# Kernel optimization log

Measured on AMD Instinct MI355X. Metric: run time of the kernel, lower is better.

Reference implementation:

```python
import jax, jax.numpy as jnp
import numpy as np

NEI = 15  # module hard-codes 15 neighbors per node via reshape(N, 15, 2)


def setup_inputs() -> dict:
    N = 10000
    # 15-regular symmetric circulant graph: offsets +-1..+-7 and +N/2 (its own inverse).
    offsets = np.array(list(range(1, 8)) + list(range(-7, 0)) + [N // 2], dtype=np.int64)
    cols = (np.arange(N)[:, None] + offsets[None, :]) % N  # (N, 15)
    adj = np.zeros((N, N), dtype=np.float32)
    adj[np.repeat(np.arange(N), NEI), cols.ravel()] = 1.0
    return {"adjacency_matrix": jnp.asarray(adj)}


def reference(adjacency_matrix):
    N = adjacency_matrix.shape[0]
    # Exactly 15 nonzeros per row -> static size N*15; row-major order matches
    # torch .nonzero(), so reshape gives per-row neighbor columns.
    _, cols = jnp.nonzero(adjacency_matrix, size=N * NEI)
    nb1 = cols.reshape(N, NEI)            # (N,15)   neighbors_one_indexes
    nb2 = nb1[nb1]                        # (N,15,15)  neighbors_two_indexes
    nb3 = nb1[nb2]                        # (N,15,15,15) neighbors_three_indexes
    # closed 3-walk: l-th neighbor of k equals the start node i
    closed = nb3 == jnp.arange(N)[:, None, None, None]
    i, j, k, l = jnp.nonzero(closed)      # data-dependent count (eager)
    # triangles_indexes_test[:, :3] == (i, nb1[i,j], nb2[i,j,k]); temp_l is dropped
    tri = jnp.stack((i, nb1[i, j], nb2[i, j, k]), axis=1)
    tri_sorted = jnp.sort(tri, axis=-1)
    triangles_ids_igraph = jnp.unique(tri_sorted, axis=0)
    return triangles_ids_igraph
```

## Files before the change

### kernel.cpp

```cpp
#include <hip/hip_runtime.h>
#include <math.h>

#define NEI 15
#define ROWSTRIDE 16

typedef float f4 __attribute__((ext_vector_type(4)));

#define GET16(n0, n1, n2, n3, K)                                   \
    ((K) < 8                                                       \
         ? ((K) < 4                                                \
                ? ((K) == 0 ? (n0).x : (K) == 1 ? (n0).y           \
                                : (K) == 2 ? (n0).z : (n0).w)      \
                : ((K) == 4 ? (n1).x : (K) == 5 ? (n1).y           \
                                : (K) == 6 ? (n1).z : (n1).w))     \
         : ((K) < 12                                               \
                ? ((K) == 8 ? (n2).x : (K) == 9 ? (n2).y           \
                                : (K) == 10 ? (n2).z : (n2).w)     \
                : ((K) == 12 ? (n3).x : (K) == 13 ? (n3).y         \
                                : (K) == 14 ? (n3).z : (n3).w)))

__device__ __forceinline__ int mbcnt64(unsigned long long m) {
    int c = __builtin_amdgcn_mbcnt_lo((unsigned)m, 0);
    c = __builtin_amdgcn_mbcnt_hi((unsigned)(m >> 32), c);
    return c;
}

__global__ void find_nb_kernel(const float* __restrict__ A,
                               int* __restrict__ nb, int N, int totalWaves) {
    const int wavesPerBlock = blockDim.x >> 6;
    const int waveId = blockIdx.x * wavesPerBlock + (threadIdx.x >> 6);
    const int lane = threadIdx.x & 63;
    const int n4 = N >> 2;

    for (int row = waveId; row < N; row += totalWaves) {
        const f4* rowp = reinterpret_cast<const f4*>(A + (long long)row * N);
        int count = 0;

        for (int c0 = 0; c0 < n4; c0 += 256) {
            const int i0 = c0 + lane;
            const int i1 = i0 + 64, i2 = i0 + 128, i3 = i0 + 192;
            f4 v0 = {0.f, 0.f, 0.f, 0.f}, v1 = {0.f, 0.f, 0.f, 0.f};
            f4 v2 = {0.f, 0.f, 0.f, 0.f}, v3 = {0.f, 0.f, 0.f, 0.f};
            if (i0 < n4) v0 = __builtin_nontemporal_load(&rowp[i0]);
            if (i1 < n4) v1 = __builtin_nontemporal_load(&rowp[i1]);
            if (i2 < n4) v2 = __builtin_nontemporal_load(&rowp[i2]);
            if (i3 < n4) v3 = __builtin_nontemporal_load(&rowp[i3]);

            const bool a0 = (v0.x != 0.f) || (v0.y != 0.f) || (v0.z != 0.f) || (v0.w != 0.f);
            const bool a1 = (v1.x != 0.f) || (v1.y != 0.f) || (v1.z != 0.f) || (v1.w != 0.f);
            const bool a2 = (v2.x != 0.f) || (v2.y != 0.f) || (v2.z != 0.f) || (v2.w != 0.f);
            const bool a3 = (v3.x != 0.f) || (v3.y != 0.f) || (v3.z != 0.f) || (v3.w != 0.f);
            if (__ballot(a0 || a1 || a2 || a3) == 0ull) continue;

            #pragma unroll
            for (int q = 0; q < 4; ++q) {
                const f4 v = (q == 0) ? v0 : (q == 1) ? v1 : (q == 2) ? v2 : v3;
                const int idx = c0 + q * 64 + lane;
                const unsigned long long m0 = __ballot(v.x != 0.f);
                const unsigned long long m1 = __ballot(v.y != 0.f);
                const unsigned long long m2 = __ballot(v.z != 0.f);
                const unsigned long long m3 = __ballot(v.w != 0.f);
                if ((m0 | m1 | m2 | m3) != 0ull) {
                    const int below = mbcnt64(m0) + mbcnt64(m1) + mbcnt64(m2) + mbcnt64(m3);
                    const int b0 = (int)((m0 >> lane) & 1ull);
                    const int b1 = (int)((m1 >> lane) & 1ull);
                    const int b2 = (int)((m2 >> lane) & 1ull);
                    const int base = count + below;
                    if (v.x != 0.f) { const int p = base;                if (p < NEI) nb[row * ROWSTRIDE + p] = (idx << 2) + 0; }
                    if (v.y != 0.f) { const int p = base + b0;           if (p < NEI) nb[row * ROWSTRIDE + p] = (idx << 2) + 1; }
                    if (v.z != 0.f) { const int p = base + b0 + b1;      if (p < NEI) nb[row * ROWSTRIDE + p] = (idx << 2) + 2; }
                    if (v.w != 0.f) { const int p = base + b0 + b1 + b2; if (p < NEI) nb[row * ROWSTRIDE + p] = (idx << 2) + 3; }
                    count += __popcll(m0) + __popcll(m1) + __popcll(m2) + __popcll(m3);
                }
            }
        }
        const int base4 = n4 << 2;
        const int rem = N - base4;
        if (rem > 0) {
            float v = 0.f;
            if (lane < rem) v = A[(long long)row * N + base4 + lane];
            const unsigned long long m = __ballot(v != 0.f);
            if (v != 0.f) {
                const int p = count + mbcnt64(m);
                if (p < NEI) nb[row * ROWSTRIDE + p] = base4 + lane;
            }
        }
    }
}

__global__ void count_tri_kernel(const int* __restrict__ nb,
                                 int* __restrict__ mask2,
                                 int* __restrict__ offs2,
                                 int* __restrict__ blockSums, int N) {
    __shared__ int partial[256];
    const int tid = blockIdx.x * 256 + threadIdx.x;
    const int M = N * NEI;
    int c = 0, mask = 0;
    if (tid < M) {
        const int i = tid / NEI;
        const int j = tid - i * NEI;
        const int a = nb[i * ROWSTRIDE + j];
        if (a > i) {
            const int4* np = reinterpret_cast<const int4*>(nb + a * ROWSTRIDE);
            const int4 n0 = np[0], n1 = np[1], n2 = np[2], n3 = np[3];
            const int4* vp = reinterpret_cast<const int4*>(nb + i * ROWSTRIDE);
            const int4 w0 = vp[0], w1 = vp[1], w2 = vp[2], w3 = vp[3];
            #pragma unroll
            for (int k = 1; k < NEI; ++k) {
                if (k > j) {
                    const int b = GET16(w0, w1, w2, w3, k);
                    const bool adj =
                        (n0.x == b) || (n0.y == b) || (n0.z == b) || (n0.w == b) ||
                        (n1.x == b) || (n1.y == b) || (n1.z == b) || (n1.w == b) ||
                        (n2.x == b) || (n2.y == b) || (n2.z == b) || (n2.w == b) ||
                        (n3.x == b) || (n3.y == b) || (n3.z == b);
                    if (adj) { mask |= (1 << k); ++c; }
                }
            }
        }
        mask2[tid] = mask;
    }
    partial[threadIdx.x] = c;
    __syncthreads();
    #pragma unroll
    for (int d = 1; d < 256; d <<= 1) {
        const int mine  = partial[threadIdx.x];
        const int other = (threadIdx.x >= d) ? partial[threadIdx.x - d] : 0;
        __syncthreads();
        partial[threadIdx.x] = mine + other;
        __syncthreads();
    }
    if (tid < M) offs2[tid] = (threadIdx.x == 0) ? 0 : partial[threadIdx.x - 1];
    if (threadIdx.x == 255) blockSums[blockIdx.x] = partial[255];
}

__global__ void scan2_kernel(const int* __restrict__ blockSums,
                             int* __restrict__ blockOffs, int B) {
    __shared__ int partial[256];
    const int tid = threadIdx.x;
    const int per = (B + 255) / 256;
    const int start = tid * per;
    int s = 0;
    for (int q = 0; q < per; ++q) {
        const int idx = start + q;
        if (idx < B) s += blockSums[idx];
    }
    partial[tid] = s;
    __syncthreads();
    #pragma unroll
    for (int d = 1; d < 256; d <<= 1) {
        const int mine  = partial[tid];
        const int other = (tid >= d) ? partial[tid - d] : 0;
        __syncthreads();
        partial[tid] = mine + other;
        __syncthreads();
    }
    int run = (tid == 0) ? 0 : partial[tid - 1];
    for (int q = 0; q < per; ++q) {
        const int idx = start + q;
        if (idx < B) { blockOffs[idx] = run; run += blockSums[idx]; }
    }
}

__global__ void emit_tri_kernel(const int* __restrict__ nb,
                                const int* __restrict__ mask2,
                                const int* __restrict__ offs2,
                                const int* __restrict__ blockOffs,
                                int* __restrict__ out, int N) {
    const int tid = blockIdx.x * blockDim.x + threadIdx.x;
    const int M = N * NEI;
    if (tid >= M) return;
    const int mask = mask2[tid];
    if (mask == 0) return;
    const int i = tid / NEI;
    const int j = tid - i * NEI;
    const int a = nb[i * ROWSTRIDE + j];
    const int4* vp = reinterpret_cast<const int4*>(nb + i * ROWSTRIDE);
    const int4 w0 = vp[0], w1 = vp[1], w2 = vp[2], w3 = vp[3];
    int pos = offs2[tid] + blockOffs[tid >> 8];
    #pragma unroll
    for (int k = 1; k < NEI; ++k) {
        if ((mask >> k) & 1) {
            const int b = GET16(w0, w1, w2, w3, k);
            out[3 * pos + 0] = i;
            out[3 * pos + 1] = a;
            out[3 * pos + 2] = b;
            ++pos;
        }
    }
}

extern "C" void kernel_launch(void* const* d_in, const int* in_sizes, int n_in,
                              void* d_out, int out_size, void* d_ws, size_t ws_size,
                              hipStream_t stream) {
    const float* A = (const float*)d_in[0];
    const long long total = (long long)in_sizes[0];
    const int N = (int)llround(sqrt((double)total));
    const int M = N * NEI;
    const int B = (M + 255) / 256;

    int* ws = (int*)d_ws;
    int* w_nb    = ws;
    int* w_mask2 = ws + N * ROWSTRIDE;
    int* w_offs2 = w_mask2 + M;
    int* w_bsum  = w_offs2 + M;
    int* w_boff  = w_bsum + B;

    int* out = (int*)d_out;

    {
        int totalWaves = (N <= 8192) ? N : (N + 1) / 2;
        const int blocks = (totalWaves + 3) / 4;
        totalWaves = blocks * 4;
        find_nb_kernel<<<blocks, 256, 0, stream>>>(A, w_nb, N, totalWaves);
    }
    count_tri_kernel<<<B, 256, 0, stream>>>(w_nb, w_mask2, w_offs2, w_bsum, N);
    scan2_kernel<<<1, 256, 0, stream>>>(w_bsum, w_boff, B);
    {
        const int threads = 256;
        const int blocks = (M + threads - 1) / threads;
        emit_tri_kernel<<<blocks, threads, 0, stream>>>(w_nb, w_mask2, w_offs2, w_boff, out, N);
    }
}
```

Measured before the change: 76.89 us.

## Fuse count, scan and emit into one single-pass decoupled-lookback kernel

Replaces the separate count, block-scan and emit kernels with one kernel. It computes per-block triangle counts, resolves the global offset with a decoupled lookback over per-block status flags, then writes triangles directly from registers. Flag state is zeroed inside the first kernel. This removes two launches and the mask and offset round-trips through global memory. In exchange, blocks spin waiting on their predecessors, which relies on blocks being scheduled in order.

```diff
diff --git a/kernel.cpp b/kernel.cpp
--- a/kernel.cpp
+++ b/kernel.cpp
@@ -3,6 +3,10 @@
 
 #define NEI 15
 #define ROWSTRIDE 16
+
+#define FLAG_INVALID 0
+#define FLAG_AGG     1
+#define FLAG_PREFIX  2
 
 typedef float f4 __attribute__((ext_vector_type(4)));
 
@@ -26,7 +30,12 @@
 }
 
 __global__ void find_nb_kernel(const float* __restrict__ A,
-                               int* __restrict__ nb, int N, int totalWaves) {
+                               int* __restrict__ nb,
+                               int* __restrict__ state, int nState,
+                               int N, int totalWaves) {
+    if (blockIdx.x == 0) {
+        for (int q = threadIdx.x; q < nState; q += blockDim.x) state[q] = 0;
+    }
     const int wavesPerBlock = blockDim.x >> 6;
     const int waveId = blockIdx.x * wavesPerBlock + (threadIdx.x >> 6);
     const int lane = threadIdx.x & 63;
@@ -88,23 +97,25 @@
     }
 }
 
-__global__ void count_tri_kernel(const int* __restrict__ nb,
-                                 int* __restrict__ mask2,
-                                 int* __restrict__ offs2,
-                                 int* __restrict__ blockSums, int N) {
+__global__ __launch_bounds__(256) void tri_kernel(const int* __restrict__ nb,
+                                                  int* __restrict__ state,
+                                                  int* __restrict__ out, int N) {
     __shared__ int partial[256];
+    __shared__ int s_prefix;
     const int tid = blockIdx.x * 256 + threadIdx.x;
     const int M = N * NEI;
-    int c = 0, mask = 0;
+
+    int c = 0, mask = 0, i = 0, j = 0, a = 0;
+    int4 w0 = {0,0,0,0}, w1 = {0,0,0,0}, w2 = {0,0,0,0}, w3 = {0,0,0,0};
     if (tid < M) {
-        const int i = tid / NEI;
-        const int j = tid - i * NEI;
-        const int a = nb[i * ROWSTRIDE + j];
+        i = tid / NEI;
+        j = tid - i * NEI;
+        a = nb[i * ROWSTRIDE + j];
         if (a > i) {
             const int4* np = reinterpret_cast<const int4*>(nb + a * ROWSTRIDE);
             const int4 n0 = np[0], n1 = np[1], n2 = np[2], n3 = np[3];
             const int4* vp = reinterpret_cast<const int4*>(nb + i * ROWSTRIDE);
-            const int4 w0 = vp[0], w1 = vp[1], w2 = vp[2], w3 = vp[3];
+            w0 = vp[0]; w1 = vp[1]; w2 = vp[2]; w3 = vp[3];
             #pragma unroll
             for (int k = 1; k < NEI; ++k) {
                 if (k > j) {
@@ -118,8 +129,8 @@
                 }
             }
         }
-        mask2[tid] = mask;
-    }
+    }
+
     partial[threadIdx.x] = c;
     __syncthreads();
     #pragma unroll
@@ -130,62 +141,68 @@
         partial[threadIdx.x] = mine + other;
         __syncthreads();
     }
-    if (tid < M) offs2[tid] = (threadIdx.x == 0) ? 0 : partial[threadIdx.x - 1];
-    if (threadIdx.x == 255) blockSums[blockIdx.x] = partial[255];
-}
-
-__global__ void scan2_kernel(const int* __restrict__ blockSums,
-                             int* __restrict__ blockOffs, int B) {
-    __shared__ int partial[256];
-    const int tid = threadIdx.x;
-    const int per = (B + 255) / 256;
-    const int start = tid * per;
-    int s = 0;
-    for (int q = 0; q < per; ++q) {
-        const int idx = start + q;
-        if (idx < B) s += blockSums[idx];
-    }
-    partial[tid] = s;
+    const int localExcl  = (threadIdx.x == 0) ? 0 : partial[threadIdx.x - 1];
+    const int blockTotal = partial[255];
+
+    if (threadIdx.x == 0) {
+        const int flag = (blockIdx.x == 0) ? FLAG_PREFIX : FLAG_AGG;
+        __hip_atomic_store(&state[blockIdx.x], (blockTotal << 2) | flag,
+                           __ATOMIC_RELEASE, __HIP_MEMORY_SCOPE_AGENT);
+        if (blockIdx.x == 0) s_prefix = 0;
+    }
+
+    if (blockIdx.x > 0 && threadIdx.x < 64) {
+        const int lane = threadIdx.x;
+        int excl = 0;
+        int windowHi = blockIdx.x;
+        while (true) {
+            const int idx = windowHi - 64 + lane;
+            int st = FLAG_PREFIX;
+            if (idx >= 0)
+                st = __hip_atomic_load(&state[idx], __ATOMIC_ACQUIRE,
+                                       __HIP_MEMORY_SCOPE_AGENT);
+            const int flag = st & 3;
+            const unsigned long long pmask = __ballot(flag == FLAG_PREFIX);
+            const unsigned long long vmask = __ballot(flag != FLAG_INVALID);
+            if (pmask != 0ull) {
+                const int hp = 63 - __clzll(pmask);
+                const unsigned long long need =
+                    (hp == 0) ? ~0ull : ~((1ull << hp) - 1ull);
+                if ((vmask & need) == need) {
+                    int contrib = (lane >= hp) ? (st >> 2) : 0;
+                    #pragma unroll
+                    for (int d = 32; d >= 1; d >>= 1) contrib += __shfl_xor(contrib, d);
+                    excl += contrib;
+                    if (lane == 0) {
+                        s_prefix = excl;
+                        __hip_atomic_store(&state[blockIdx.x],
+                                           ((excl + blockTotal) << 2) | FLAG_PREFIX,
+                                           __ATOMIC_RELEASE, __HIP_MEMORY_SCOPE_AGENT);
+                    }
+                    break;
+                }
+            } else if (vmask == ~0ull) {
+                int contrib = st >> 2;
+                #pragma unroll
+                for (int d = 32; d >= 1; d >>= 1) contrib += __shfl_xor(contrib, d);
+                excl += contrib;
+                windowHi -= 64;
+            }
+        }
+    }
     __syncthreads();
-    #pragma unroll
-    for (int d = 1; d < 256; d <<= 1) {
-        const int mine  = partial[tid];
-        const int other = (tid >= d) ? partial[tid - d] : 0;
-        __syncthreads();
-        partial[tid] = mine + other;
-        __syncthreads();
-    }
-    int run = (tid == 0) ? 0 : partial[tid - 1];
-    for (int q = 0; q < per; ++q) {
-        const int idx = start + q;
-        if (idx < B) { blockOffs[idx] = run; run += blockSums[idx]; }
-    }
-}
-
-__global__ void emit_tri_kernel(const int* __restrict__ nb,
-                                const int* __restrict__ mask2,
-                                const int* __restrict__ offs2,
-                                const int* __restrict__ blockOffs,
-                                int* __restrict__ out, int N) {
-    const int tid = blockIdx.x * blockDim.x + threadIdx.x;
-    const int M = N * NEI;
-    if (tid >= M) return;
-    const int mask = mask2[tid];
-    if (mask == 0) return;
-    const int i = tid / NEI;
-    const int j = tid - i * NEI;
-    const int a = nb[i * ROWSTRIDE + j];
-    const int4* vp = reinterpret_cast<const int4*>(nb + i * ROWSTRIDE);
-    const int4 w0 = vp[0], w1 = vp[1], w2 = vp[2], w3 = vp[3];
-    int pos = offs2[tid] + blockOffs[tid >> 8];
-    #pragma unroll
-    for (int k = 1; k < NEI; ++k) {
-        if ((mask >> k) & 1) {
-            const int b = GET16(w0, w1, w2, w3, k);
-            out[3 * pos + 0] = i;
-            out[3 * pos + 1] = a;
-            out[3 * pos + 2] = b;
-            ++pos;
+
+    if (tid < M && mask != 0) {
+        int pos = s_prefix + localExcl;
+        #pragma unroll
+        for (int k = 1; k < NEI; ++k) {
+            if ((mask >> k) & 1) {
+                const int b = GET16(w0, w1, w2, w3, k);
+                out[3 * pos + 0] = i;
+                out[3 * pos + 1] = a;
+                out[3 * pos + 2] = b;
+                ++pos;
+            }
         }
     }
 }
@@ -197,14 +214,11 @@
     const long long total = (long long)in_sizes[0];
     const int N = (int)llround(sqrt((double)total));
     const int M = N * NEI;
-    const int B = (M + 255) / 256;
+    const int B2 = (M + 255) / 256;
 
     int* ws = (int*)d_ws;
     int* w_nb    = ws;
-    int* w_mask2 = ws + N * ROWSTRIDE;
-    int* w_offs2 = w_mask2 + M;
-    int* w_bsum  = w_offs2 + M;
-    int* w_boff  = w_bsum + B;
+    int* w_state = ws + N * ROWSTRIDE;
 
     int* out = (int*)d_out;
 
@@ -212,13 +226,7 @@
         int totalWaves = (N <= 8192) ? N : (N + 1) / 2;
         const int blocks = (totalWaves + 3) / 4;
         totalWaves = blocks * 4;
-        find_nb_kernel<<<blocks, 256, 0, stream>>>(A, w_nb, N, totalWaves);
-    }
-    count_tri_kernel<<<B, 256, 0, stream>>>(w_nb, w_mask2, w_offs2, w_bsum, N);
-    scan2_kernel<<<1, 256, 0, stream>>>(w_bsum, w_boff, B);
-    {
-        const int threads = 256;
-        const int blocks = (M + threads - 1) / threads;
-        emit_tri_kernel<<<blocks, threads, 0, stream>>>(w_nb, w_mask2, w_offs2, w_boff, out, N);
-    }
-}
+        find_nb_kernel<<<blocks, 256, 0, stream>>>(A, w_nb, w_state, B2, N, totalWaves);
+    }
+    tri_kernel<<<B2, 256, 0, stream>>>(w_nb, w_state, out, N);
+}
```

Result: slower. 112.8 us (+46.7%).
